# Optimization experiments

Measured on AMD Instinct MI355X. Metric: run time of the kernel, lower is better.

Reference implementation:

```python
import jax, jax.numpy as jnp
import numpy as np

VOCAB = 50000
EMB = 64
HID = 64


def _lstm_final(emb_t, mask_t, W, U, b):
    # emb_t: (T, B, EMB), mask_t: (T, B) bool. Keras gate order: i, f, g(c), o.
    B = emb_t.shape[1]
    h0 = jnp.zeros((B, HID), emb_t.dtype)
    c0 = jnp.zeros((B, HID), emb_t.dtype)

    def step(carry, xm):
        h, c = carry
        x, m = xm
        z = x @ W + h @ U + b  # (B, 4H)
        i, f, g, o = jnp.split(z, 4, axis=-1)
        i = jax.nn.sigmoid(i)
        f = jax.nn.sigmoid(f)
        g = jnp.tanh(g)
        o = jax.nn.sigmoid(o)
        c_new = f * c + i * g
        h_new = o * jnp.tanh(c_new)
        m = m[:, None]
        h = jnp.where(m, h_new, h)  # masked steps carry state through
        c = jnp.where(m, c_new, c)
        return (h, c), None

    (h, c), _ = jax.lax.scan(step, (h0, c0), (emb_t, mask_t))
    return h


def setup_inputs() -> dict:
    key = jax.random.key(0)
    ks = jax.random.split(key, 12)
    B, T = 512, 1024
    x = jax.random.randint(ks[0], (B, T), 0, VOCAB + 1, dtype=jnp.int64)
    s = 0.05
    inp = {
        "x": x,
        "emb_table": jax.random.normal(ks[1], (VOCAB + 1, EMB), jnp.float32) * s,
        "Wf": jax.random.normal(ks[2], (EMB, 4 * HID), jnp.float32) * s,
        "Uf": jax.random.normal(ks[3], (HID, 4 * HID), jnp.float32) * s,
        "bf": jnp.zeros((4 * HID,), jnp.float32),
        "Wb": jax.random.normal(ks[4], (EMB, 4 * HID), jnp.float32) * s,
        "Ub": jax.random.normal(ks[5], (HID, 4 * HID), jnp.float32) * s,
        "bb": jnp.zeros((4 * HID,), jnp.float32),
        "W1": jax.random.normal(ks[6], (2 * HID, 32), jnp.float32) * s,
        "b1": jnp.zeros((32,), jnp.float32),
        "W2": jax.random.normal(ks[7], (32, 1), jnp.float32) * s,
        "b2": jnp.zeros((1,), jnp.float32),
    }
    return inp


def reference(x, emb_table, Wf, Uf, bf, Wb, Ub, bb, W1, b1, W2, b2):
    mask = x != 0  # (B, T) mask_zero
    emb = emb_table[x]  # (B, T, EMB)
    emb_t = jnp.transpose(emb, (1, 0, 2))  # (T, B, EMB)
    mask_t = jnp.transpose(mask, (1, 0))   # (T, B)
    h_fwd = _lstm_final(emb_t, mask_t, Wf, Uf, bf)
    h_bwd = _lstm_final(emb_t[::-1], mask_t[::-1], Wb, Ub, bb)
    h = jnp.concatenate([h_fwd, h_bwd], axis=-1)  # (B, 2H)
    h = jax.nn.relu(h @ W1 + b1)  # dropout is identity at inference
    out = h @ W2 + b2  # (B, 1)
    return out
```

## Files before the change

### kernel.cpp

```cpp
#include <hip/hip_runtime.h>

#define T 1024
#define BATCH 512
#define EMB 64
#define HID 64
#define NGATE 256
#define VOCABP1 50001

typedef unsigned int uint32;
typedef unsigned short u16;
typedef __attribute__((ext_vector_type(8))) short short8;
typedef __attribute__((ext_vector_type(4))) float f32x4;
typedef __attribute__((ext_vector_type(4))) float float4v;

#define L2E 1.44269504088896340736f

__device__ __forceinline__ float rcpf(float x) { return __builtin_amdgcn_rcpf(x); }
__device__ __forceinline__ float exp2as(float x) {
    float r;
    asm("v_exp_f32 %0, %1" : "=v"(r) : "v"(x));
    return r;
}
__device__ __forceinline__ float sigm_pre(float z)  { return rcpf(1.0f + exp2as(z)); }
__device__ __forceinline__ float tanh_pre(float z)  { return fmaf(-2.0f, rcpf(exp2as(z) + 1.0f), 1.0f); }
__device__ __forceinline__ float tanh_c(float c)    { return tanh_pre(c * (2.0f * L2E)); }

__device__ __forceinline__ u16 f2bf(float x) {
    uint32 u = __float_as_uint(x);
    u += 0x7fffu + ((u >> 16) & 1u);
    return (u16)(u >> 16);
}
__device__ __forceinline__ float bf2f(u16 h) { return __uint_as_float(((uint32)h) << 16); }

#define BARRIER_LDS() asm volatile("s_waitcnt lgkmcnt(0)\n\ts_barrier" ::: "memory")

__global__ void prep_kernel(const int* __restrict__ x, const float* __restrict__ emb,
                            const float* __restrict__ Uf, const float* __restrict__ Ub,
                            const float* __restrict__ Wf, const float* __restrict__ Wb,
                            u16* __restrict__ xstream, uint32* __restrict__ mbits,
                            u16* __restrict__ bfrag)
{
    const int bid = blockIdx.x;
    const int tid = threadIdx.x;

    if (bid < 2048) {
        const int gb    = bid >> 6;
        const int stile = bid & 63;
        const int lane  = tid & 63;
        const int half  = tid >> 6;
        const int ks    = half & 1;
        const int sp    = half >> 1;
        const int m     = lane & 15;
        const int qj    = (lane >> 4) * 8;
#pragma unroll
        for (int i = 0; i < 8; ++i) {
            const int s   = stile * 16 + sp * 8 + i;
            const int tok = x[(gb * 16 + m) * T + s];
            const float* er = emb + (size_t)tok * EMB + ks * 32 + qj;
            const float4v a = *(const float4v*)er;
            const float4v b = *(const float4v*)(er + 4);
            short8 v;
            v[0] = (short)f2bf(a[0]); v[1] = (short)f2bf(a[1]);
            v[2] = (short)f2bf(a[2]); v[3] = (short)f2bf(a[3]);
            v[4] = (short)f2bf(b[0]); v[5] = (short)f2bf(b[1]);
            v[6] = (short)f2bf(b[2]); v[7] = (short)f2bf(b[3]);
            *(short8*)(xstream + ((size_t)(gb * 1024 + s) * 128 + ks * 64 + lane) * 8) = v;
        }
    } else if (bid < 2048 + 128) {
        const int idx  = (bid - 2048) * 256 + tid;
        const int word = idx & 31;
        const int db   = idx >> 5;
        const int d    = db >> 9;
        const int b    = db & 511;
        const int* src = x + b * T;
        uint32 m = 0;
#pragma unroll 8
        for (int i = 0; i < 32; ++i) {
            const int t = word * 32 + i;
            m |= (src[d ? (T - 1 - t) : t] != 0 ? 1u : 0u) << i;
        }
        mbits[idx] = m;
    } else {
        const int bid3 = bid - 2176;
        const int d  = bid3 >> 3;
        const int g  = (bid3 >> 1) & 3;
        const int ks = bid3 & 1;
        const float* U = d ? Ub : Uf;
        const float* W = d ? Wb : Wf;
        const int lane = tid & 63, w = tid >> 6;
        const float scale = (g == 2) ? (2.0f * L2E) : (-L2E);
#pragma unroll
        for (int j = 0; j < 8; ++j) {
            const int col = g * 64 + 16 * w + (lane & 15);
            const int k   = ks * 32 + (lane >> 4) * 8 + j;
            const float uv = U[k * NGATE + col] * scale;
            const u16 uhi = f2bf(uv);
            const u16 ulo = f2bf(uv - bf2f(uhi));
            const u16 whi = f2bf(W[k * NGATE + col] * scale);
            const size_t base = ((((size_t)(d * 4 + w) * 4 + g) * 2 + ks) * 3) * 512;
            bfrag[base + 0 * 512 + lane * 8 + j] = uhi;
            bfrag[base + 1 * 512 + lane * 8 + j] = ulo;
            bfrag[base + 2 * 512 + lane * 8 + j] = whi;
        }
    }
}

__global__ __launch_bounds__(256, 1)
void lstm_mfma(const uint32* __restrict__ mbits,
               const u16* __restrict__ xstream,
               const u16* __restrict__ bfragp,
               const float* __restrict__ bf, const float* __restrict__ bb,
               float* __restrict__ hcat)
{
    const int tid  = threadIdx.x;
    const int lane = tid & 63;
    const int w    = tid >> 6;
    const int col  = lane & 15;
    const int quad = lane >> 4;
    const int gb16  = blockIdx.x & 31;
    const int inner = blockIdx.x >> 5;
    const int d     = inner >> 2;
    const int sub   = inner & 3;

    const int ucol = 16 * w + col;
    const int KS   = w >> 1;

    short8 BUh[4][2];
    short8 BW[4][2];
    {
        const u16* pb = bfragp + (size_t)(d * 4 + w) * 4 * 2 * 3 * 512;
#pragma unroll
        for (int g = 0; g < 4; ++g)
#pragma unroll
        for (int ks = 0; ks < 2; ++ks) {
            BUh[g][ks] = *(const short8*)&pb[((g * 2 + ks) * 3 + 0) * 512 + lane * 8];
            BW[g][ks]  = *(const short8*)&pb[((g * 2 + ks) * 3 + 2) * 512 + lane * 8];
        }
    }
    float biasv[4];
    {
        const float* bias = d ? bb : bf;
#pragma unroll
        for (int g = 0; g < 4; ++g)
            biasv[g] = bias[g * 64 + ucol] * ((g == 2) ? (2.0f * L2E) : (-L2E));
    }

    __shared__ u16 Ahl[2][2][64][8];
    {
        u16* f = &Ahl[0][0][0][0];
        for (int i = tid; i < 2 * 2 * 64 * 8; i += 256) f[i] = 0;
    }

    const uint32* mrow = mbits + (size_t)(d * 512 + gb16 * 16 + 4 * sub + quad) * 32;
    uint32 mcur = mrow[0], mnext = mrow[1];
    const int q2u  = (2 * w + (col >> 3)) & 3;
    const int hrow = q2u * 16 + 4 * quad;
    const int hj   = col & 7;

    const u16* sptr = xstream + (size_t)gb16 * 1024 * 1024;

    const int srcoff    = ((lane & 48) | (4 * sub + ((lane & 15) >> 2))) * 8;
    const int lanedelta = srcoff + (d ? -(lane & 3) : (lane & 3)) * 1024;

#define XBATCH(XT, G)                                                          \
    XT[G][0] = biasv[G]; XT[G][1] = biasv[G];                                  \
    XT[G][2] = biasv[G]; XT[G][3] = biasv[G];                                  \
    XT[G] = __builtin_amdgcn_mfma_f32_16x16x32_bf16(axr[0], BW[G][0], XT[G], 0, 0, 0); \
    XT[G] = __builtin_amdgcn_mfma_f32_16x16x32_bf16(axr[1], BW[G][1], XT[G], 0, 0, 0);

    short8 axr[2];
    f32x4  xaccA[4], xaccB[4];
    {
        const int c2 = d ? 1023 : 0;
        const u16* cp = sptr + (size_t)c2 * 1024;
        axr[0] = *(const short8*)(cp + lanedelta);
        axr[1] = *(const short8*)(cp + 512 + lanedelta);
        XBATCH(xaccA, 0) XBATCH(xaccA, 1) XBATCH(xaccA, 2) XBATCH(xaccA, 3)
    }
    f32x4 xinit[4];
#pragma unroll
    for (int g = 0; g < 4; ++g) { xinit[g][0] = 0.f; xinit[g][1] = 0.f; xinit[g][2] = 0.f; xinit[g][3] = 0.f; }

    __syncthreads();

    float hv = 0.f, cv = 0.f;

#define STEP(SV, P, XC, XP, QP)                                                \
  {                                                                            \
    if ((QP) == 0) {        \
      const int cs = ((SV) + 4 <= 1020) ? ((SV) + 4) : 1020;                   \
      const int c2 = d ? (1023 - cs) : cs;                                     \
      const u16* cp = sptr + (size_t)c2 * 1024;                                \
      axr[0] = *(const short8*)(cp + lanedelta);                               \
      axr[1] = *(const short8*)(cp + 512 + lanedelta);                         \
      if ((((SV) & 31) == 0) && ((SV) > 0)) {                                  \
        const int wn = ((SV) >> 5) + 1;                                        \
        const int wc = (wn < 32) ? wn : 31;                                    \
        mcur = mnext; mnext = mrow[wc];                                        \
      }                                                                        \
    }                                                                          \
    BARRIER_LDS();                                                             \
    const short8 Ah0 = *(const short8*)&Ahl[1 - (P)][0][lane][0];              \
    const short8 Ah1 = *(const short8*)&Ahl[1 - (P)][1][lane][0];              \
                  \
    xinit[0][0] = XC[0][(QP)];                                                 \
    xinit[1][0] = XC[1][(QP)];                                                 \
    xinit[2][0] = XC[2][(QP)];                                                 \
    xinit[3][0] = XC[3][(QP)];                                                 \
    if ((QP) == 2) { XBATCH(XP, 0) XBATCH(XP, 1) }                             \
    if ((QP) == 3) { XBATCH(XP, 2) XBATCH(XP, 3) }                             \
    \
    f32x4 a2 = __builtin_amdgcn_mfma_f32_16x16x32_bf16(Ah0, BUh[2][0], xinit[2], 0, 0, 0); \
    a2       = __builtin_amdgcn_mfma_f32_16x16x32_bf16(Ah1, BUh[2][1], a2, 0, 0, 0);       \
    f32x4 a0 = __builtin_amdgcn_mfma_f32_16x16x32_bf16(Ah0, BUh[0][0], xinit[0], 0, 0, 0); \
    a0       = __builtin_amdgcn_mfma_f32_16x16x32_bf16(Ah1, BUh[0][1], a0, 0, 0, 0);       \
    f32x4 a1 = __builtin_amdgcn_mfma_f32_16x16x32_bf16(Ah0, BUh[1][0], xinit[1], 0, 0, 0); \
    a1       = __builtin_amdgcn_mfma_f32_16x16x32_bf16(Ah1, BUh[1][1], a1, 0, 0, 0);       \
    f32x4 a3 = __builtin_amdgcn_mfma_f32_16x16x32_bf16(Ah0, BUh[3][0], xinit[3], 0, 0, 0); \
    a3       = __builtin_amdgcn_mfma_f32_16x16x32_bf16(Ah1, BUh[3][1], a3, 0, 0, 0);       \
         \
    {                                                                          \
      const float gg = a2[0] + a2[1];                                          \
      const float gv = tanh_pre(gg);                                           \
      const float gi = a0[0] + a0[1];                                          \
      const float iv = sigm_pre(gi);                                           \
      const float gf = a1[0] + a1[1];                                          \
      const float fv = sigm_pre(gf);                                           \
      const float ig = iv * gv;                                                \
      const float cn = fmaf(fv, cv, ig);                                       \
      const float go = a3[0] + a3[1];                                          \
      const float ov = sigm_pre(go);                                           \
      const float th = tanh_c(cn);                                             \
      const float hn = ov * th;                                                \
      if ((mcur >> ((SV) & 31)) & 1) { cv = cn; hv = hn; }                     \
      const uint32 uh = __float_as_uint(hv);                                   \
      const u16 hhi = (u16)(uh >> 16);                                         \
      const u16 hlo = (u16)(__float_as_uint(hv - bf2f(hhi)) >> 16);            \
      Ahl[(P)][KS][hrow][hj]     = hhi;                                        \
      Ahl[(P)][KS][hrow + 1][hj] = hlo;                                        \
    }                                                                          \
  }

    for (int s = 0; s < T; s += 8) {
        STEP(s,     0, xaccA, xaccB, 0)
        STEP(s + 1, 1, xaccA, xaccB, 1)
        STEP(s + 2, 0, xaccA, xaccB, 2)
        STEP(s + 3, 1, xaccA, xaccB, 3)
        STEP(s + 4, 0, xaccB, xaccA, 0)
        STEP(s + 5, 1, xaccB, xaccA, 1)
        STEP(s + 6, 0, xaccB, xaccA, 2)
        STEP(s + 7, 1, xaccB, xaccA, 3)
    }
#undef STEP
#undef XBATCH

    hcat[(size_t)(gb16 * 16 + 4 * sub + quad) * (2 * HID) + d * HID + ucol] = hv;
}

__global__ void mlp_kernel(const float* __restrict__ hcat,
                           const float* __restrict__ W1, const float* __restrict__ b1,
                           const float* __restrict__ W2, const float* __restrict__ b2,
                           float* __restrict__ out)
{
    const int b   = blockIdx.x;
    const int tid = threadIdx.x;
    const int m   = tid & 31;
    const int kh  = tid >> 5;
    __shared__ float part[2][32];
    const float* h = hcat + b * (2 * HID);

    float acc = (kh == 0) ? b1[m] : 0.0f;
#pragma unroll
    for (int k = 0; k < 64; ++k) acc += h[kh * 64 + k] * W1[(kh * 64 + k) * 32 + m];
    part[kh][m] = acc;
    __syncthreads();
    if (tid < 32) {
        const float h1 = fmaxf(part[0][tid] + part[1][tid], 0.0f);
        float v = h1 * W2[tid];
#pragma unroll
        for (int o = 16; o > 0; o >>= 1) v += __shfl_down(v, o);
        if (tid == 0) out[b] = v + b2[0];
    }
}

extern "C" void kernel_launch(void* const* d_in, const int* in_sizes, int n_in,
                              void* d_out, int out_size, void* d_ws, size_t ws_size,
                              hipStream_t stream)
{
    const int*   x   = (const int*)d_in[0];
    const float* emb = (const float*)d_in[1];
    const float* Wf  = (const float*)d_in[2];
    const float* Uf  = (const float*)d_in[3];
    const float* bf  = (const float*)d_in[4];
    const float* Wb  = (const float*)d_in[5];
    const float* Ub  = (const float*)d_in[6];
    const float* bb  = (const float*)d_in[7];
    const float* W1  = (const float*)d_in[8];
    const float* b1  = (const float*)d_in[9];
    const float* W2  = (const float*)d_in[10];
    const float* b2  = (const float*)d_in[11];
    float* out = (float*)d_out;

    u16*    xstream = (u16*)d_ws;
    uint32* mbits   = (uint32*)(xstream + (size_t)32 * 1024 * 1024);
    u16*    bfragp  = (u16*)(mbits + 2 * 512 * 32);
    float*  hcat    = (float*)(bfragp + 98304);

    prep_kernel<<<dim3(2048 + 128 + 16), dim3(256), 0, stream>>>(
        x, emb, Uf, Ub, Wf, Wb, xstream, mbits, bfragp);
    lstm_mfma<<<dim3(256), dim3(256), 0, stream>>>(mbits, xstream, bfragp, bf, bb, hcat);
    mlp_kernel<<<dim3(BATCH), dim3(64), 0, stream>>>(hcat, W1, b1, W2, b2, out);
}
```

Measured before the change: 379.2 us.

## Fuse MLP head into LSTM kernel via last-block atomic flag, vectorize token loads

Removes the separate MLP kernel launch. Each LSTM block increments a per-group counter after writing its hidden state, and the second block to finish (fwd/bwd pair) computes the dense head for its four sequences using LDS scratch. A prep block zeroes the flags each call. The embedding gather also reads tokens as two int4 vector loads instead of eight scalar loads. The change adds threadfence and atomic overhead to the recurrent kernel's tail.

```diff
diff --git a/kernel.cpp b/kernel.cpp
--- a/kernel.cpp
+++ b/kernel.cpp
@@ -12,6 +12,7 @@
 typedef __attribute__((ext_vector_type(8))) short short8;
 typedef __attribute__((ext_vector_type(4))) float f32x4;
 typedef __attribute__((ext_vector_type(4))) float float4v;
+typedef __attribute__((ext_vector_type(4))) int int4v;
 
 #define L2E 1.44269504088896340736f
 
@@ -38,7 +39,7 @@
                             const float* __restrict__ Uf, const float* __restrict__ Ub,
                             const float* __restrict__ Wf, const float* __restrict__ Wb,
                             u16* __restrict__ xstream, uint32* __restrict__ mbits,
-                            u16* __restrict__ bfrag)
+                            u16* __restrict__ bfrag, uint32* __restrict__ flags)
 {
     const int bid = blockIdx.x;
     const int tid = threadIdx.x;
@@ -52,10 +53,13 @@
         const int sp    = half >> 1;
         const int m     = lane & 15;
         const int qj    = (lane >> 4) * 8;
+        const int4v* xp = (const int4v*)(x + (gb * 16 + m) * T + stile * 16 + sp * 8);
+        const int4v t0 = xp[0];
+        const int4v t1 = xp[1];
 #pragma unroll
         for (int i = 0; i < 8; ++i) {
             const int s   = stile * 16 + sp * 8 + i;
-            const int tok = x[(gb * 16 + m) * T + s];
+            const int tok = (i < 4) ? t0[i & 3] : t1[i & 3];
             const float* er = emb + (size_t)tok * EMB + ks * 32 + qj;
             const float4v a = *(const float4v*)er;
             const float4v b = *(const float4v*)(er + 4);
@@ -80,7 +84,7 @@
             m |= (src[d ? (T - 1 - t) : t] != 0 ? 1u : 0u) << i;
         }
         mbits[idx] = m;
-    } else {
+    } else if (bid < 2048 + 128 + 16) {
         const int bid3 = bid - 2176;
         const int d  = bid3 >> 3;
         const int g  = (bid3 >> 1) & 3;
@@ -102,6 +106,8 @@
             bfrag[base + 1 * 512 + lane * 8 + j] = ulo;
             bfrag[base + 2 * 512 + lane * 8 + j] = whi;
         }
+    } else {
+        if (tid < 128) flags[tid] = 0;
     }
 }
 
@@ -110,7 +116,10 @@
                const u16* __restrict__ xstream,
                const u16* __restrict__ bfragp,
                const float* __restrict__ bf, const float* __restrict__ bb,
-               float* __restrict__ hcat)
+               float* __restrict__ hcat, uint32* __restrict__ flags,
+               const float* __restrict__ W1, const float* __restrict__ b1,
+               const float* __restrict__ W2, const float* __restrict__ b2,
+               float* __restrict__ out)
 {
     const int tid  = threadIdx.x;
     const int lane = tid & 63;
@@ -255,31 +264,32 @@
 #undef XBATCH
 
     hcat[(size_t)(gb16 * 16 + 4 * sub + quad) * (2 * HID) + d * HID + ucol] = hv;
-}
-
-__global__ void mlp_kernel(const float* __restrict__ hcat,
-                           const float* __restrict__ W1, const float* __restrict__ b1,
-                           const float* __restrict__ W2, const float* __restrict__ b2,
-                           float* __restrict__ out)
-{
-    const int b   = blockIdx.x;
-    const int tid = threadIdx.x;
-    const int m   = tid & 31;
-    const int kh  = tid >> 5;
-    __shared__ float part[2][32];
-    const float* h = hcat + b * (2 * HID);
-
-    float acc = (kh == 0) ? b1[m] : 0.0f;
-#pragma unroll
-    for (int k = 0; k < 64; ++k) acc += h[kh * 64 + k] * W1[(kh * 64 + k) * 32 + m];
-    part[kh][m] = acc;
+
+    __threadfence();
+    __shared__ uint32 winls;
+    if (tid == 0) winls = atomicAdd(&flags[gb16 * 4 + sub], 1u);
     __syncthreads();
-    if (tid < 32) {
-        const float h1 = fmaxf(part[0][tid] + part[1][tid], 0.0f);
-        float v = h1 * W2[tid];
-#pragma unroll
-        for (int o = 16; o > 0; o >>= 1) v += __shfl_down(v, o);
-        if (tid == 0) out[b] = v + b2[0];
+    if (winls == 1) {
+        __threadfence();
+        float* part = (float*)&Ahl[0][0][0][0];
+        const int p  = tid >> 6;
+        const int m  = tid & 31;
+        const int kh = (tid >> 5) & 1;
+        const int seq = gb16 * 16 + 4 * sub + p;
+        const float* h = hcat + (size_t)seq * (2 * HID);
+        float acc = (kh == 0) ? b1[m] : 0.0f;
+#pragma unroll
+        for (int k = 0; k < 64; ++k)
+            acc += h[kh * 64 + k] * W1[(kh * 64 + k) * 32 + m];
+        part[(p * 2 + kh) * 32 + m] = acc;
+        __syncthreads();
+        if ((tid & 63) < 32) {
+            const float h1 = fmaxf(part[(p * 2) * 32 + m] + part[(p * 2 + 1) * 32 + m], 0.0f);
+            float v = h1 * W2[m];
+#pragma unroll
+            for (int o = 16; o > 0; o >>= 1) v += __shfl_down(v, o, 32);
+            if (m == 0) out[seq] = v + b2[0];
+        }
     }
 }
 
@@ -305,9 +315,10 @@
     uint32* mbits   = (uint32*)(xstream + (size_t)32 * 1024 * 1024);
     u16*    bfragp  = (u16*)(mbits + 2 * 512 * 32);
     float*  hcat    = (float*)(bfragp + 98304);
-
-    prep_kernel<<<dim3(2048 + 128 + 16), dim3(256), 0, stream>>>(
-        x, emb, Uf, Ub, Wf, Wb, xstream, mbits, bfragp);
-    lstm_mfma<<<dim3(256), dim3(256), 0, stream>>>(mbits, xstream, bfragp, bf, bb, hcat);
-    mlp_kernel<<<dim3(BATCH), dim3(64), 0, stream>>>(hcat, W1, b1, W2, b2, out);
-}
+    uint32* flags   = (uint32*)(hcat + 512 * 128);
+
+    prep_kernel<<<dim3(2048 + 128 + 16 + 1), dim3(256), 0, stream>>>(
+        x, emb, Uf, Ub, Wf, Wb, xstream, mbits, bfragp, flags);
+    lstm_mfma<<<dim3(256), dim3(256), 0, stream>>>(
+        mbits, xstream, bfragp, bf, bb, hcat, flags, W1, b1, W2, b2, out);
+}
```

After: 398.6 us. +5.1%, slower.
